# Kernel optimization log

Measured on AMD Instinct MI355X. Metric: run time of the kernel, lower is better.

Reference implementation:

```python
import jax, jax.numpy as jnp
import numpy as np

ALPHA = 0.7            # _cfg.alpha  (abnormal-growth threshold ratio)
SIGMA = 0.1            # _cfg.sigma  (gaussian splatting bandwidth)
MIN_MINING_STEP = 50   # _cfg.min_mining_step
NCROPS = 2             # pfu crop count (uncrop = mean over crops)


def setup_inputs() -> dict:
    key = jax.random.key(0)
    k1, k2 = jax.random.split(key)
    B, T, C = 64, 2048, NCROPS
    scores = jax.random.normal(k1, (B * C, T), dtype=jnp.float32)
    # balanced bag: first half abnormal (labels==1), matching bat_div == bs//2
    labels = jnp.concatenate([jnp.ones(B // 2, jnp.int32), jnp.zeros(B // 2, jnp.int32)])
    point_label = (jax.random.uniform(k2, (B, T)) < 0.004).astype(jnp.int32)
    seqlen = jnp.full((B,), T, dtype=jnp.int32)  # full length -> no padding path
    return {"scores": scores, "labels": labels, "point_label": point_label,
            "seqlen": seqlen, "step": 100}


def _mine_one(score, plabel, valid_len):
    """gaussian_kernel_mining for one video. score/plabel: [T].
    Grows labels outward from each anchor while score >= ALPHA*score[anchor],
    stopping at the first failure (segmented cumulative-AND, resetting at anchors)."""
    T = score.shape[0]
    is_anchor = plabel > 0

    def scan_dir(s, a):
        def step(carry, xs):
            ok, anch, has = carry          # chain-unbroken flag, last anchor score, anchor seen
            sj, aj = xs
            cond = sj >= ALPHA * anch
            grown = ok & cond & has        # position mined by growth in this direction
            ok2 = jnp.where(aj, True, grown)
            anch2 = jnp.where(aj, sj, anch)
            return (ok2, anch2, has | aj), grown
        init = (jnp.asarray(True), jnp.float32(0.0), jnp.asarray(False))
        _, g = jax.lax.scan(step, init, (s, a))
        return g

    g_fwd = scan_dir(score, is_anchor) & (jnp.arange(T) < valid_len)  # rightward growth
    g_bwd = scan_dir(score[::-1], is_anchor[::-1])[::-1]              # leftward growth
    return (is_anchor | g_fwd | g_bwd).astype(jnp.float32)


def _splat_table(T):
    """[p, i] normalized gaussian weights; identical for every video since N==T."""
    i = jnp.arange(T, dtype=jnp.float32)
    h = 2.0 * (i - 1.0) / (T - 1.0) - 1.0
    d = h[None, :] - h[:, None]
    W = jnp.exp(-d * d / (2.0 * SIGMA * SIGMA)) / (SIGMA * jnp.sqrt(2.0 * jnp.pi))
    wmin = W.min(axis=1, keepdims=True)
    wmax = W.max(axis=1, keepdims=True)
    return jnp.where(wmax > wmin, (W - wmin) / (wmax - wmin), jnp.ones_like(W))


def _splat_one(mask, Wn):
    """temporal_gaussian_splatting for one video: max over anchor rows, then min-max."""
    any_a = mask.any()
    temp = jnp.max(jnp.where(mask[:, None], Wn, -jnp.inf), axis=0)
    tmin, tmax = temp.min(), temp.max()
    temp_n = jnp.where(tmax > tmin, (temp - tmin) / (tmax - tmin), temp)
    return jnp.where(any_a, temp_n, jnp.zeros_like(temp))


def reference(scores, labels, point_label, seqlen, step):
    BC, T = scores.shape
    B = BC // NCROPS
    nb = B // 2  # bat_div == bs//2: first half abnormal
    # sigmoid then uncrop (mean over crops)
    probs = jax.nn.sigmoid(scores).reshape(B, NCROPS, T).mean(axis=1)
    abn_scores = probs[:nb]                      # unbag abnormal half
    abn_pl = point_label[:nb]
    # mining runs on detached scores -> pseudo labels carry no gradient
    s_det = jax.lax.stop_gradient(abn_scores)
    abn_kernel = jax.vmap(_mine_one)(s_det, abn_pl, seqlen[:nb])
    base = abn_pl.astype(jnp.float32) if step < MIN_MINING_STEP else abn_kernel
    Wn = _splat_table(T)
    rendered = jax.vmap(lambda m: _splat_one(m > 0, Wn))(base)
    # BCELoss(reduction='none').mean() with rendered as target
    per_elem = -(rendered * jnp.log(abn_scores) + (1.0 - rendered) * jnp.log1p(-abn_scores))
    return jnp.mean(per_elem)
```

## Files before the change

kernel.cpp:

```cpp
#include <hip/hip_runtime.h>
#include <cstdint>
#include <climits>
#include <cmath>

#define ALPHA 0.7f
#define SIGMA 0.1f
#define MIN_MINING_STEP 50

constexpr int TT    = 2048;
constexpr int NTH   = 256;
constexpr int EPT   = TT / NTH;
constexpr int NWAVE = NTH / 64;

__device__ __forceinline__ void dual_maxscan(int (&v)[EPT], int (&w)[EPT],
                                             int& exV, int& exW, int* sW) {
    const int tid = threadIdx.x, lane = tid & 63, wid = tid >> 6;
#pragma unroll
    for (int k = 1; k < EPT; ++k) {
        v[k] = max(v[k], v[k - 1]);
        w[k] = max(w[k], w[k - 1]);
    }
    int tv = v[EPT - 1], tw = w[EPT - 1];
#pragma unroll
    for (int off = 1; off < 64; off <<= 1) {
        int nv = __shfl_up(tv, off), nw = __shfl_up(tw, off);
        if (lane >= off) { tv = max(tv, nv); tw = max(tw, nw); }
    }
    if (lane == 63) { sW[wid] = tv; sW[NWAVE + wid] = tw; }
    __syncthreads();
    int ev = INT_MIN, ew = INT_MIN;
    for (int q = 0; q < wid; ++q) {
        ev = max(ev, sW[q]);
        ew = max(ew, sW[NWAVE + q]);
    }
    int uv = __shfl_up(tv, 1), uw = __shfl_up(tw, 1);
    if (lane > 0) { ev = max(ev, uv); ew = max(ew, uw); }
    exV = ev; exW = ew;
#pragma unroll
    for (int k = 0; k < EPT; ++k) {
        v[k] = max(v[k], ev);
        w[k] = max(w[k], ew);
    }
    __syncthreads();
}

__device__ __forceinline__ float waveRedMin(float v) {
#pragma unroll
    for (int off = 32; off > 0; off >>= 1) v = fminf(v, __shfl_xor(v, off));
    return v;
}
__device__ __forceinline__ float waveRedSum(float v) {
#pragma unroll
    for (int off = 32; off > 0; off >>= 1) v += __shfl_xor(v, off);
    return v;
}

__global__ __launch_bounds__(NTH) void glance_fused(
    const float* __restrict__ scores,
    const int*   __restrict__ point_label,
    const int*   __restrict__ seqlen,
    const int*   __restrict__ step_p,
    float*        wsF,
    unsigned int* wsC,
    float* __restrict__ out,
    int C, int nb, float invN)
{
    __shared__ float sS[TT];
    __shared__ int   sM[TT];
    __shared__ int   sW[2 * NWAVE];
    __shared__ float sR[NWAVE];
    __shared__ int   sAny;

    const int b = blockIdx.x, tid = threadIdx.x, lane = tid & 63, wid = tid >> 6;

    const float invC = 1.0f / (float)C;
    for (int q4 = tid; q4 < TT / 4; q4 += NTH) {
        float4 acc = make_float4(0.f, 0.f, 0.f, 0.f);
        for (int c = 0; c < C; ++c) {
            const float4 x = ((const float4*)(scores + ((size_t)(b * C + c)) * TT))[q4];
            acc.x += 1.0f / (1.0f + __expf(-x.x));
            acc.y += 1.0f / (1.0f + __expf(-x.y));
            acc.z += 1.0f / (1.0f + __expf(-x.z));
            acc.w += 1.0f / (1.0f + __expf(-x.w));
        }
        const int4 p = ((const int4*)(point_label + (size_t)b * TT))[q4];
        const int t = q4 * 4;
        sS[t + 0] = acc.x * invC;  sM[t + 0] = (p.x > 0) ? 1 : 0;
        sS[t + 1] = acc.y * invC;  sM[t + 1] = (p.y > 0) ? 1 : 0;
        sS[t + 2] = acc.z * invC;  sM[t + 2] = (p.z > 0) ? 1 : 0;
        sS[t + 3] = acc.w * invC;  sM[t + 3] = (p.w > 0) ? 1 : 0;
    }
    const int stepv = step_p[0];
    const int vlen  = seqlen[b];
    __syncthreads();

    const int j0 = tid * EPT;

    if (stepv >= MIN_MINING_STEP) {
        int va[EPT], wa[EPT]; int exA, exB;
#pragma unroll
        for (int k = 0; k < EPT; ++k) {
            const int j = j0 + k;
            va[k] = sM[j] ? j : -1;
            wa[k] = sM[TT - 1 - j] ? j : -1;
        }
        dual_maxscan(va, wa, exA, exB, sW);

        int vf[EPT], wf[EPT]; int exF, exG;
        int qf[EPT], qb[EPT];
#pragma unroll
        for (int k = 0; k < EPT; ++k) {
            const int j  = j0 + k;
            const int qF = (k == 0) ? exA : va[k - 1];
            const int qB = (k == 0) ? exB : wa[k - 1];
            qf[k] = qF; qb[k] = qB;
            bool cF = false, cB = false;
            if (qF >= 0) cF = sS[j]          >= ALPHA * sS[qF];
            if (qB >= 0) cB = sS[TT - 1 - j] >= ALPHA * sS[TT - 1 - qB];
            vf[k] = cF ? -1 : j;
            wf[k] = cB ? -1 : j;
        }
        dual_maxscan(vf, wf, exF, exG, sW);

#pragma unroll
        for (int k = 0; k < EPT; ++k) {
            const int j = j0 + k;
            const bool gF = (qf[k] >= 0) && (vf[k] <= qf[k]) && (j < vlen);
            const bool gB = (qb[k] >= 0) && (wf[k] <= qb[k]);
            if (gF) sM[j] = 1;
            if (gB) sM[TT - 1 - j] = 1;
        }
        __syncthreads();
    }

    int vn[EPT], wn[EPT]; int exN, exO;
#pragma unroll
    for (int k = 0; k < EPT; ++k) {
        const int j = j0 + k;
        vn[k] = sM[j] ? j : -1;
        wn[k] = sM[TT - 1 - j] ? j : -1;
    }
    dual_maxscan(vn, wn, exN, exO, sW);

#pragma unroll
    for (int k = 0; k < EPT; ++k) {
        const int j  = j0 + k;
        const int dB = (wn[k] >= 0) ? min(j - wn[k], 4096) : 4096;
        sM[TT - 1 - j] = dB;
    }
    if (tid == NTH - 1) sAny = (vn[EPT - 1] >= 0) ? 1 : 0;
    __syncthreads();

    const float KK = 2.0f / ((float)(TT - 1) * (float)(TT - 1) * SIGMA * SIGMA);
    float tempv[EPT];
    float tmn = INFINITY;
#pragma unroll
    for (int k = 0; k < EPT; ++k) {
        const int j  = j0 + k;
        const int dF = (vn[k] >= 0) ? min(j - vn[k], 4096) : 4096;
        const int d  = min(dF, sM[j]);
        const float tv = __expf(-KK * (float)(d * d));
        tempv[k] = tv;
        tmn = fminf(tmn, tv);
    }
    tmn = waveRedMin(tmn);
    if (lane == 0) sR[wid] = tmn;
    __syncthreads();
    tmn = sR[0];
    for (int w = 1; w < NWAVE; ++w) tmn = fminf(tmn, sR[w]);
    __syncthreads();

    const bool any  = (sAny != 0);
    const bool norm = any && (tmn < 1.0f);
    const float inv = norm ? 1.0f / (1.0f - tmn) : 0.0f;
    float lsum = 0.0f;
#pragma unroll
    for (int k = 0; k < EPT; ++k) {
        float r = 0.0f;
        if (any) r = norm ? (tempv[k] - tmn) * inv : tempv[k];
        const float s = sS[j0 + k];
        lsum += -(r * __logf(s) + (1.0f - r) * __logf(1.0f - s));
    }
    lsum = waveRedSum(lsum);
    if (lane == 0) sR[wid] = lsum;
    __syncthreads();

    if (tid == 0) {
        float tot = 0.0f;
        for (int w = 0; w < NWAVE; ++w) tot += sR[w];
        atomicAdd(wsF, tot);
        __threadfence();
        const unsigned int c = atomicAdd(wsC, 1u);
        if (c == (unsigned int)(nb - 1)) {
            const float total = atomicAdd(wsF, 0.0f);
            out[0] = total * invN;
        }
    }
}

extern "C" void kernel_launch(void* const* d_in, const int* in_sizes, int n_in,
                              void* d_out, int out_size, void* d_ws, size_t ws_size,
                              hipStream_t stream) {
    (void)n_in; (void)out_size; (void)ws_size;
    const float* scores      = (const float*)d_in[0];
    const int*   point_label = (const int*)d_in[2];
    const int*   seqlen      = (const int*)d_in[3];
    const int*   step_p      = (const int*)d_in[4];

    const int B  = in_sizes[1];
    const int T  = in_sizes[2] / B;
    const int C  = in_sizes[0] / (B * T);
    const int nb = B / 2;

    float*        wsF = (float*)d_ws;
    unsigned int* wsC = (unsigned int*)d_ws + 1;
    hipMemsetAsync(d_ws, 0, 8, stream);

    glance_fused<<<nb, NTH, 0, stream>>>(scores, point_label, seqlen, step_p,
                                         wsF, wsC, (float*)d_out,
                                         C, nb, 1.0f / (float)(nb * T));
}
```

Measured before the change: 69.91 us.

## Double block size, drop scan barriers, replace atomics with second reduce kernel

Doubles the threads per block so each thread scans 4 elements instead of 8. Removes the trailing barrier in the max-scan helper by giving each scan its own shared-memory slot. Drops the memset, global atomics and last-block detection, and instead writes per-block partial sums that a small second kernel reduces. This trades a memset and an atomic counter for an extra kernel launch. The 64-thread reduce kernel assumes nb is at most 64.

```diff
diff --git a/kernel.cpp b/kernel.cpp
--- a/kernel.cpp
+++ b/kernel.cpp
@@ -8,7 +8,7 @@
 #define MIN_MINING_STEP 50
 
 constexpr int TT    = 2048;
-constexpr int NTH   = 256;
+constexpr int NTH   = 512;
 constexpr int EPT   = TT / NTH;
 constexpr int NWAVE = NTH / 64;
 
@@ -41,7 +41,6 @@
         v[k] = max(v[k], ev);
         w[k] = max(w[k], ew);
     }
-    __syncthreads();
 }
 
 __device__ __forceinline__ float waveRedMin(float v) {
@@ -60,16 +59,14 @@
     const int*   __restrict__ point_label,
     const int*   __restrict__ seqlen,
     const int*   __restrict__ step_p,
-    float*        wsF,
-    unsigned int* wsC,
-    float* __restrict__ out,
-    int C, int nb, float invN)
+    float*       __restrict__ partial,
+    int C)
 {
     __shared__ float sS[TT];
     __shared__ int   sM[TT];
-    __shared__ int   sW[2 * NWAVE];
-    __shared__ float sR[NWAVE];
-    __shared__ int   sAny;
+    __shared__ int   sW[6 * NWAVE];
+    __shared__ float sRmin[NWAVE];
+    __shared__ float sRsum[NWAVE];
 
     const int b = blockIdx.x, tid = threadIdx.x, lane = tid & 63, wid = tid >> 6;
 
@@ -120,7 +117,7 @@
             vf[k] = cF ? -1 : j;
             wf[k] = cB ? -1 : j;
         }
-        dual_maxscan(vf, wf, exF, exG, sW);
+        dual_maxscan(vf, wf, exF, exG, sW + 2 * NWAVE);
 
 #pragma unroll
         for (int k = 0; k < EPT; ++k) {
@@ -140,7 +137,7 @@
         vn[k] = sM[j] ? j : -1;
         wn[k] = sM[TT - 1 - j] ? j : -1;
     }
-    dual_maxscan(vn, wn, exN, exO, sW);
+    dual_maxscan(vn, wn, exN, exO, sW + 4 * NWAVE);
 
 #pragma unroll
     for (int k = 0; k < EPT; ++k) {
@@ -148,8 +145,9 @@
         const int dB = (wn[k] >= 0) ? min(j - wn[k], 4096) : 4096;
         sM[TT - 1 - j] = dB;
     }
-    if (tid == NTH - 1) sAny = (vn[EPT - 1] >= 0) ? 1 : 0;
-    __syncthreads();
+    if (tid == NTH - 1) sW[0] = (vn[EPT - 1] >= 0) ? 1 : 0;
+    __syncthreads();
+    const bool any = (sW[0] != 0);
 
     const float KK = 2.0f / ((float)(TT - 1) * (float)(TT - 1) * SIGMA * SIGMA);
     float tempv[EPT];
@@ -164,13 +162,11 @@
         tmn = fminf(tmn, tv);
     }
     tmn = waveRedMin(tmn);
-    if (lane == 0) sR[wid] = tmn;
-    __syncthreads();
-    tmn = sR[0];
-    for (int w = 1; w < NWAVE; ++w) tmn = fminf(tmn, sR[w]);
-    __syncthreads();
-
-    const bool any  = (sAny != 0);
+    if (lane == 0) sRmin[wid] = tmn;
+    __syncthreads();
+    tmn = sRmin[0];
+    for (int w = 1; w < NWAVE; ++w) tmn = fminf(tmn, sRmin[w]);
+
     const bool norm = any && (tmn < 1.0f);
     const float inv = norm ? 1.0f / (1.0f - tmn) : 0.0f;
     float lsum = 0.0f;
@@ -182,20 +178,22 @@
         lsum += -(r * __logf(s) + (1.0f - r) * __logf(1.0f - s));
     }
     lsum = waveRedSum(lsum);
-    if (lane == 0) sR[wid] = lsum;
-    __syncthreads();
-
+    if (lane == 0) sRsum[wid] = lsum;
+    __syncthreads();
     if (tid == 0) {
         float tot = 0.0f;
-        for (int w = 0; w < NWAVE; ++w) tot += sR[w];
-        atomicAdd(wsF, tot);
-        __threadfence();
-        const unsigned int c = atomicAdd(wsC, 1u);
-        if (c == (unsigned int)(nb - 1)) {
-            const float total = atomicAdd(wsF, 0.0f);
-            out[0] = total * invN;
-        }
-    }
+        for (int w = 0; w < NWAVE; ++w) tot += sRsum[w];
+        partial[b] = tot;
+    }
+}
+
+__global__ __launch_bounds__(64) void glance_reduce(
+    const float* __restrict__ partial, float* __restrict__ out, int nb, float invN)
+{
+    float v = ((int)threadIdx.x < nb) ? partial[threadIdx.x] : 0.0f;
+#pragma unroll
+    for (int off = 32; off > 0; off >>= 1) v += __shfl_down(v, off);
+    if (threadIdx.x == 0) out[0] = v * invN;
 }
 
 extern "C" void kernel_launch(void* const* d_in, const int* in_sizes, int n_in,
@@ -212,11 +210,10 @@
     const int C  = in_sizes[0] / (B * T);
     const int nb = B / 2;
 
-    float*        wsF = (float*)d_ws;
-    unsigned int* wsC = (unsigned int*)d_ws + 1;
-    hipMemsetAsync(d_ws, 0, 8, stream);
+    float* partial = (float*)d_ws;
 
     glance_fused<<<nb, NTH, 0, stream>>>(scores, point_label, seqlen, step_p,
-                                         wsF, wsC, (float*)d_out,
-                                         C, nb, 1.0f / (float)(nb * T));
-}
+                                         partial, C);
+    glance_reduce<<<1, 64, 0, stream>>>(partial, (float*)d_out, nb,
+                                        1.0f / (float)(nb * T));
+}
```

Result: faster. 67.82 us (-3.0%).
